# Kernel optimization log

Hardware: AMD Instinct MI355X
Metric: run time of the kernel (lower is better)

Reference implementation:

```python
import jax, jax.numpy as jnp
import numpy as np

B, L, T, D1, D2, H = 4096, 50, 100, 128, 128, 4
NUM_USERS, NUM_ITEMS = 100000, 100000
STEP = 1
NEG_INF = -9e15


def setup_inputs() -> dict:
    key = jax.random.key(0)
    ks = jax.random.split(key, 17)
    xav = lambda k, shape: jax.random.uniform(k, shape, jnp.float32,
                                              -np.sqrt(6.0 / (shape[0] + shape[1])),
                                              np.sqrt(6.0 / (shape[0] + shape[1])))
    return {
        # int inputs
        "item_seq": jax.random.randint(ks[0], (B, L), 0, NUM_ITEMS),
        "user_ids": jax.random.randint(ks[1], (B,), 0, NUM_USERS),
        "items_to_predict": jax.random.randint(ks[2], (B, T), 0, NUM_ITEMS),
        "A": jax.random.randint(ks[3], (B, L, L), 0, 2).astype(jnp.int32),
        # embedding tables (normal_(0, 1/dim) as in torch init)
        "item_emb_table": jax.random.normal(ks[4], (NUM_ITEMS, D1), jnp.float32) / D1,
        "user_emb_table": jax.random.normal(ks[5], (NUM_USERS, D2), jnp.float32) / D2,
        "W2_table": jax.random.normal(ks[6], (NUM_ITEMS, D1), jnp.float32) / D1,
        "b2_table": jnp.zeros((NUM_ITEMS, 1), jnp.float32),
        # GAT params (one head layer + output layer), xavier_uniform
        "W_att": xav(ks[7], (D1, D1)),
        "a_att": xav(ks[8], (2 * D1, 1)),
        "W_out": xav(ks[9], (D1, D1)),
        "a_out": xav(ks[10], (2 * D1, 1)),
        # item-attention MLP (torch Linear stored as [in, out] + bias)
        "att1_W": xav(ks[11], (D1, D1)),
        "att1_b": jnp.zeros((D1,), jnp.float32),
        "att2_W": xav(ks[12], (D1, H)),
        "att2_b": jnp.zeros((H,), jnp.float32),
        "user_com": xav(ks[13], (D1 + D2, D1)),
    }


def _gat_layer(x, adj, W, a, concat):
    # x: [B,L,Fin], adj: [B,L,L]
    h = jnp.einsum("blf,fg->blg", x, W)            # [B,L,F]
    F_out = W.shape[1]
    a1, a2 = a[:F_out, 0], a[F_out:, 0]
    # e[b,i,j] = tanh(h_i . a1 + h_j . a2) -- equivalent to the pairwise concat
    f1 = h @ a1                                     # [B,L]
    f2 = h @ a2                                     # [B,L]
    e = jnp.tanh(f1[:, :, None] + f2[:, None, :])   # [B,L,L]
    att = jnp.where(adj > 0, e, NEG_INF)
    att = jax.nn.softmax(att, axis=2)
    h_prime = jnp.einsum("bij,bjf->bif", att, h)
    return jax.nn.elu(h_prime) if concat else h_prime


def reference(item_seq, user_ids, items_to_predict, A,
              item_emb_table, user_emb_table, W2_table, b2_table,
              W_att, a_att, W_out, a_out,
              att1_W, att1_b, att2_W, att2_b, user_com):
    item_embs = item_emb_table[item_seq]            # [B,L,D1]
    user_emb = user_emb_table[user_ids]             # [B,D2]

    # GAT (nb_heads=1, so the head concat is identity)
    x = item_embs
    for _ in range(STEP):
        x = _gat_layer(x, A, W_att, a_att, concat=True)
        x = jax.nn.elu(_gat_layer(x, A, W_out, a_out, concat=False))
    short_embs = x                                   # [B,L,D1]

    # multi-head item attention pooling
    m1 = jnp.tanh(short_embs @ att1_W + att1_b)      # [B,L,D1]
    m2 = m1 @ att2_W + att2_b                        # [B,L,H]
    attn = jax.nn.softmax(m2, axis=2)                # softmax over heads
    matrix_z = jnp.einsum("bld,blh->bdh", short_embs, attn)  # [B,D1,H]
    attention_embs = jnp.mean(jnp.tanh(matrix_z), axis=2)     # [B,D1]

    fusion = jnp.concatenate([attention_embs, user_emb], axis=1) @ user_com  # [B,D1]

    w2 = W2_table[items_to_predict]                  # [B,T,D1]
    b2 = b2_table[items_to_predict]                  # [B,T,1]
    res = jnp.einsum("btd,bd->bt", w2, fusion) + b2[..., 0]   # baddbmm
    rel_score = jnp.einsum("bld,btd->bt", item_embs, w2)       # sum over L
    return res + rel_score
```

## Files before the change

kernel.cpp:

```cpp
#include <hip/hip_runtime.h>
#include <math.h>

#define L_  50
#define T_  100
#define NEG_INF_ -9000000000000000.0f

using bf16x8 = __attribute__((ext_vector_type(8))) short;
using f32x4 = __attribute__((ext_vector_type(4))) float;

__device__ __forceinline__ float wred_sum(float v) {
#pragma unroll
    for (int o = 32; o > 0; o >>= 1) v += __shfl_xor(v, o, 64);
    return v;
}
__device__ __forceinline__ short f2bf(float f) {
    unsigned u = __float_as_uint(f);
    return (short)((u + 0x7fffu + ((u >> 16) & 1u)) >> 16);
}
__device__ __forceinline__ unsigned short f2bfu(float f) {
    unsigned u = __float_as_uint(f);
    return (unsigned short)((u + 0x7fffu + ((u >> 16) & 1u)) >> 16);
}
__device__ __forceinline__ float bf2f(unsigned short u) {
    return __uint_as_float(((unsigned)u) << 16);
}
__device__ __forceinline__ float tanh_fast(float x) {
    const float cx = fminf(fmaxf(x, -15.f), 15.f);
    const float t = __expf(2.f * cx);
    return (t - 1.f) * __builtin_amdgcn_rcpf(t + 1.f);
}

extern "C" __global__ void __launch_bounds__(256) magnn_preswizzle(
    const float* __restrict__ W0, const float* __restrict__ W1,
    const float* __restrict__ W2, const float* __restrict__ a0,
    const float* __restrict__ a1v, unsigned short* __restrict__ out) {
    const int t = blockIdx.x * 256 + threadIdx.x;
    const int gid = t >> 6, lane = t & 63;
    if (gid >= 104) return;
    int mat, kt, nt;
    size_t base;
    if (gid < 72) {
        mat = gid / 36;
        const int rem = gid % 36;
        kt = rem / 9;
        nt = rem % 9;
        base = (size_t)mat * 18432 + (size_t)(((kt * 9 + nt) * 64 + lane) << 3);
    } else {
        mat = 2;
        const int rem = gid - 72;
        kt = rem >> 3;
        nt = rem & 7;
        base = 36864 + (size_t)(((kt * 8 + nt) * 64 + lane) << 3);
    }
    const float* Ws = (mat == 0) ? W0 : (mat == 1) ? W1 : W2;
    const int n = lane & 15;
    const int k0 = kt * 32 + (lane >> 4) * 8;
    bf16x8 v;
    if (nt < 8) {
        const int col = nt * 16 + n;
#pragma unroll
        for (int j = 0; j < 8; ++j) v[j] = f2bf(Ws[(size_t)(k0 + j) * 128 + col]);
    } else {
        if (n < 2) {
            const float* av = ((mat == 0) ? a0 : a1v) + n * 128;
#pragma unroll
            for (int j = 0; j < 8; ++j) {
                float s = 0.f;
                const float* wr = Ws + (size_t)(k0 + j) * 128;
                for (int g = 0; g < 128; ++g) s = fmaf(wr[g], av[g], s);
                v[j] = f2bf(s);
            }
        } else {
#pragma unroll
            for (int j = 0; j < 8; ++j) v[j] = 0;
        }
    }
    *(bf16x8*)(out + base) = v;
}

__device__ __forceinline__ void gemm50_gat(
    const unsigned short* __restrict__ Wb,
    const unsigned short (&xb)[50][136], unsigned short (&ht)[128][72],
    float* __restrict__ f1s, float* __restrict__ f2s, int w, int lane) {
    const int n = lane & 15, quad = lane >> 4;
    const int mrd = w * 16 + n;
    const int mr = (mrd < 50) ? mrd : 49;
    f32x4 acc[9];
#pragma unroll
    for (int nt = 0; nt < 9; ++nt) acc[nt] = (f32x4){0.f, 0.f, 0.f, 0.f};

#pragma unroll
    for (int kt = 0; kt < 4; ++kt) {
        const bf16x8 af = *(const bf16x8*)&xb[mr][kt * 32 + quad * 8];
        const unsigned short* bp = Wb + (((kt * 9) * 64 + lane) << 3);
#pragma unroll
        for (int nt = 0; nt < 9; ++nt) {
            const bf16x8 bfr = *(const bf16x8*)(bp + (nt << 9));
            acc[nt] = __builtin_amdgcn_mfma_f32_16x16x32_bf16(af, bfr, acc[nt], 0, 0, 0);
        }
    }
    const int rbase = w * 16 + quad * 4;
#pragma unroll
    for (int nt = 0; nt < 8; ++nt) {
        const int col = nt * 16 + n;
        ushort4 pk;
        pk.x = f2bfu(acc[nt][0]);
        pk.y = f2bfu(acc[nt][1]);
        pk.z = f2bfu(acc[nt][2]);
        pk.w = f2bfu(acc[nt][3]);
        *(ushort4*)&ht[col][rbase] = pk;
    }
    if (n < 2) {
        float* fs = n ? f2s : f1s;
#pragma unroll
        for (int reg = 0; reg < 4; ++reg) fs[rbase + reg] = acc[8][reg];
    }
}

__device__ __forceinline__ void gemm_m1_m2(
    const unsigned short* __restrict__ Wb, const float* __restrict__ att1_b,
    const float* __restrict__ att2_W, const float* __restrict__ att2_b,
    const unsigned short (&xb)[50][136], float* __restrict__ attn4,
    int w, int lane) {
    const int n = lane & 15, quad = lane >> 4;
    const int mrd = w * 16 + n;
    const int mr = (mrd < 50) ? mrd : 49;
    f32x4 acc[8];
#pragma unroll
    for (int nt = 0; nt < 8; ++nt) acc[nt] = (f32x4){0.f, 0.f, 0.f, 0.f};

#pragma unroll
    for (int kt = 0; kt < 4; ++kt) {
        const bf16x8 af = *(const bf16x8*)&xb[mr][kt * 32 + quad * 8];
        const unsigned short* bp = Wb + (((kt * 8) * 64 + lane) << 3);
#pragma unroll
        for (int nt = 0; nt < 8; ++nt) {
            const bf16x8 bfr = *(const bf16x8*)(bp + (nt << 9));
            acc[nt] = __builtin_amdgcn_mfma_f32_16x16x32_bf16(af, bfr, acc[nt], 0, 0, 0);
        }
    }

    float pm[4][4];
#pragma unroll
    for (int r = 0; r < 4; ++r)
#pragma unroll
        for (int h = 0; h < 4; ++h) pm[r][h] = 0.f;

#pragma unroll
    for (int nt = 0; nt < 8; ++nt) {
        const int col = nt * 16 + n;
        const float bv = att1_b[col];
        const float4 a4 = *(const float4*)&att2_W[col * 4];
#pragma unroll
        for (int r = 0; r < 4; ++r) {
            const float tv = tanh_fast(acc[nt][r] + bv);
            pm[r][0] = fmaf(tv, a4.x, pm[r][0]);
            pm[r][1] = fmaf(tv, a4.y, pm[r][1]);
            pm[r][2] = fmaf(tv, a4.z, pm[r][2]);
            pm[r][3] = fmaf(tv, a4.w, pm[r][3]);
        }
    }
#pragma unroll
    for (int r = 0; r < 4; ++r)
#pragma unroll
        for (int h = 0; h < 4; ++h) {
            float v = pm[r][h];
            v += __shfl_xor(v, 1, 64);
            v += __shfl_xor(v, 2, 64);
            v += __shfl_xor(v, 4, 64);
            v += __shfl_xor(v, 8, 64);
            pm[r][h] = v;
        }
    if (n == 0) {
        const float ab0 = att2_b[0], ab1 = att2_b[1], ab2 = att2_b[2], ab3 = att2_b[3];
        const int rbase = w * 16 + quad * 4;
#pragma unroll
        for (int r = 0; r < 4; ++r) {
            const int row = rbase + r;
            if (row < L_) {
                const float m0 = pm[r][0] + ab0, m1 = pm[r][1] + ab1;
                const float m2 = pm[r][2] + ab2, m3 = pm[r][3] + ab3;
                const float mx = fmaxf(fmaxf(m0, m1), fmaxf(m2, m3));
                const float e0 = __expf(m0 - mx), e1 = __expf(m1 - mx);
                const float e2 = __expf(m2 - mx), e3 = __expf(m3 - mx);
                const float inv = 1.f / (e0 + e1 + e2 + e3);
                *(float4*)&attn4[row * 4] =
                    make_float4(e0 * inv, e1 * inv, e2 * inv, e3 * inv);
            }
        }
    }
}

extern "C" __global__ void __launch_bounds__(256, 4) magnn_fused(
    const int* __restrict__ iseq, const int* __restrict__ uids,
    const int* __restrict__ itp, const int* __restrict__ A,
    const float* __restrict__ item_emb, const float* __restrict__ user_emb,
    const float* __restrict__ W2t, const float* __restrict__ b2t,
    const float* __restrict__ att1_b, const float* __restrict__ att2_W,
    const float* __restrict__ att2_b, const float* __restrict__ user_com,
    const unsigned short* __restrict__ Wb, float* __restrict__ out) {
    __shared__ __align__(16) unsigned short xb[50][136];
    __shared__ __align__(16) unsigned short ht[128][72];
    __shared__ __align__(16) unsigned short Pb[50][72];
    __shared__ __align__(16) float fsc[128];
    float* f1s = fsc;
    float* f2s = fsc + 64;
    float* S = (float*)&Pb[0][0];
    float* attn4 = S;
    float* cat = S + 256;
    float* fpart = S + 512;
    float* vvec = S + 640;
    float* zpart = S + 768;

    const int tid = threadIdx.x;
    const int b = blockIdx.x;
    const int w = tid >> 6, lane = tid & 63;
    const int n16 = lane & 15, quad = lane >> 4;

    const int* Ab = A + (size_t)b * (L_ * L_);
    unsigned amask = 0;
    if (lane < L_) {
#pragma unroll
        for (int k = 0; k < 13; ++k) {
            const int l = w + 4 * k;
            if (l < L_) amask |= (Ab[l * L_ + lane] > 0) ? (1u << k) : 0u;
        }
    }

    const int* isq = iseq + b * L_;
    for (int i = tid; i < L_ * 32; i += 256) {
        const int l = i >> 5, c4 = (i & 31) << 2;
        const float4 v = *(const float4*)&item_emb[(size_t)isq[l] * 128 + c4];
        ushort4 pk;
        pk.x = f2bfu(v.x); pk.y = f2bfu(v.y); pk.z = f2bfu(v.z); pk.w = f2bfu(v.w);
        *(ushort4*)&xb[l][c4] = pk;
    }
    float sval = 0.f;
    if (tid < 128) {
#pragma unroll 10
        for (int l = 0; l < L_; ++l)
            sval += item_emb[(size_t)isq[l] * 128 + tid];
    }
    __syncthreads();

#pragma unroll 1
    for (int layer = 0; layer < 2; ++layer) {
        gemm50_gat(Wb + layer * 18432, xb, ht, f1s, f2s, w, lane);
        __syncthreads();
        {
            const float f2v = (lane < L_) ? f2s[lane] : 0.f;
#pragma unroll
            for (int k = 0; k < 13; ++k) {
                const int l = w + 4 * k;
                if (l < L_) {
                    const float e = tanh_fast(f1s[l] + f2v);
                    const float p = ((amask >> k) & 1u) ? __expf(e) : 0.f;
                    Pb[l][lane] = f2bfu(p);
                }
            }
        }
        __syncthreads();
        {
            const int pm = w * 16 + n16;
            const int pmc = (pm < 50) ? pm : 49;
            const bf16x8 pa0 = *(const bf16x8*)&Pb[pmc][quad * 8];
            const bf16x8 pa1 = *(const bf16x8*)&Pb[pmc][32 + quad * 8];
            bf16x8 bones;
#pragma unroll
            for (int j = 0; j < 8; ++j)
                bones[j] = (n16 == 0) ? (short)0x3F80 : (short)0;
            f32x4 sacc = (f32x4){0.f, 0.f, 0.f, 0.f};
            sacc = __builtin_amdgcn_mfma_f32_16x16x32_bf16(pa0, bones, sacc, 0, 0, 0);
            sacc = __builtin_amdgcn_mfma_f32_16x16x32_bf16(pa1, bones, sacc, 0, 0, 0);
            f32x4 oacc[8];
#pragma unroll
            for (int nt = 0; nt < 8; ++nt) oacc[nt] = (f32x4){0.f, 0.f, 0.f, 0.f};
#pragma unroll
            for (int nt = 0; nt < 8; ++nt) {
                const bf16x8 h0 = *(const bf16x8*)&ht[nt * 16 + n16][quad * 8];
                oacc[nt] = __builtin_amdgcn_mfma_f32_16x16x32_bf16(pa0, h0, oacc[nt], 0, 0, 0);
            }
#pragma unroll
            for (int nt = 0; nt < 8; ++nt) {
                const bf16x8 h1 = *(const bf16x8*)&ht[nt * 16 + n16][32 + quad * 8];
                oacc[nt] = __builtin_amdgcn_mfma_f32_16x16x32_bf16(pa1, h1, oacc[nt], 0, 0, 0);
            }
            float rinv[4];
#pragma unroll
            for (int reg = 0; reg < 4; ++reg) {
                const float s = __shfl(sacc[reg], (lane & 48), 64);
                rinv[reg] = __builtin_amdgcn_rcpf(s);
            }
            const int rb = w * 16 + quad * 4;
#pragma unroll
            for (int nt = 0; nt < 8; ++nt) {
#pragma unroll
                for (int reg = 0; reg < 4; ++reg) {
                    const int row = rb + reg;
                    if (row < L_) {
                        float e = oacc[nt][reg] * rinv[reg];
                        e = (e > 0.f) ? e : (__expf(e) - 1.f);
                        xb[row][nt * 16 + n16] = f2bfu(e);
                    }
                }
            }
        }
        __syncthreads();
    }

    gemm_m1_m2(Wb + 36864, att1_b, att2_W, att2_b, xb, attn4, w, lane);
    __syncthreads();

    {
        const int d = tid & 127, hf2 = tid >> 7;
        float z0 = 0.f, z1 = 0.f, z2 = 0.f, z3 = 0.f;
        const int l0 = hf2 * 25;
#pragma unroll
        for (int li = 0; li < 25; ++li) {
            const int l = l0 + li;
            const float xv = bf2f(xb[l][d]);
            const float4 at = *(const float4*)&attn4[l * 4];
            z0 = fmaf(xv, at.x, z0);
            z1 = fmaf(xv, at.y, z1);
            z2 = fmaf(xv, at.z, z2);
            z3 = fmaf(xv, at.w, z3);
        }
        if (hf2) {
            zpart[0 * 128 + d] = z0;
            zpart[1 * 128 + d] = z1;
            zpart[2 * 128 + d] = z2;
            zpart[3 * 128 + d] = z3;
            cat[128 + d] = user_emb[(size_t)uids[b] * 128 + d];
        }
        __syncthreads();
        if (!hf2) {
            z0 += zpart[0 * 128 + d];
            z1 += zpart[1 * 128 + d];
            z2 += zpart[2 * 128 + d];
            z3 += zpart[3 * 128 + d];
            cat[d] = 0.25f * (tanh_fast(z0) + tanh_fast(z1) +
                              tanh_fast(z2) + tanh_fast(z3));
        }
        __syncthreads();
    }

    {
        const int g = tid & 127, hf = tid >> 7;
        const float* ucb = user_com + hf * 128 * 128 + g;
        const float* cc = cat + hf * 128;
        float acc = 0.f;
#pragma unroll 16
        for (int k = 0; k < 128; ++k) acc = fmaf(cc[k], ucb[(size_t)k * 128], acc);
        if (hf) fpart[g] = acc;
        __syncthreads();
        if (!hf) vvec[g] = acc + fpart[g] + sval;
    }
    __syncthreads();

    {
        float vv[8];
#pragma unroll
        for (int j = 0; j < 8; ++j) vv[j] = vvec[n16 * 8 + j];
        const int* itpb = itp + b * T_;
        const int tq = w * 4 + quad;
        int ti[7];
        float bv[7];
#pragma unroll
        for (int i = 0; i < 7; ++i) {
            const int t = i * 16 + tq;
            ti[i] = itpb[(t < T_) ? t : 0];
        }
#pragma unroll
        for (int i = 0; i < 7; ++i) bv[i] = b2t[ti[i]];
#pragma unroll
        for (int i = 0; i < 7; ++i) {
            const int t = i * 16 + tq;
            const float* wr = W2t + (size_t)ti[i] * 128 + n16 * 8;
            const float4 wa = *(const float4*)wr;
            const float4 wb = *(const float4*)(wr + 4);
            float r = wa.x * vv[0];
            r = fmaf(wa.y, vv[1], r);
            r = fmaf(wa.z, vv[2], r);
            r = fmaf(wa.w, vv[3], r);
            r = fmaf(wb.x, vv[4], r);
            r = fmaf(wb.y, vv[5], r);
            r = fmaf(wb.z, vv[6], r);
            r = fmaf(wb.w, vv[7], r);
            r += __shfl_xor(r, 1, 64);
            r += __shfl_xor(r, 2, 64);
            r += __shfl_xor(r, 4, 64);
            r += __shfl_xor(r, 8, 64);
            if (n16 == 0 && t < T_) out[b * T_ + t] = r + bv[i];
        }
    }
}

extern "C" void kernel_launch(void* const* d_in, const int* in_sizes, int n_in,
                              void* d_out, int out_size, void* d_ws, size_t ws_size,
                              hipStream_t stream) {
    const int* iseq = (const int*)d_in[0];
    const int* uids = (const int*)d_in[1];
    const int* itp = (const int*)d_in[2];
    const int* A = (const int*)d_in[3];
    const float* item_emb = (const float*)d_in[4];
    const float* user_emb = (const float*)d_in[5];
    const float* W2t = (const float*)d_in[6];
    const float* b2t = (const float*)d_in[7];
    const float* W_att = (const float*)d_in[8];
    const float* a_att = (const float*)d_in[9];
    const float* W_out = (const float*)d_in[10];
    const float* a_out = (const float*)d_in[11];
    const float* att1_W = (const float*)d_in[12];
    const float* att1_b = (const float*)d_in[13];
    const float* att2_W = (const float*)d_in[14];
    const float* att2_b = (const float*)d_in[15];
    const float* user_com = (const float*)d_in[16];
    float* out = (float*)d_out;
    unsigned short* Wb = (unsigned short*)d_ws;

    magnn_preswizzle<<<dim3(26), dim3(256), 0, stream>>>(W_att, W_out, att1_W,
                                                         a_att, a_out, Wb);

    const int B = in_sizes[1];
    magnn_fused<<<dim3(B), dim3(256), 0, stream>>>(
        iseq, uids, itp, A, item_emb, user_emb, W2t, b2t, att1_b, att2_W,
        att2_b, user_com, Wb, out);
}
```

Before: 359.1 us.

## Pre-transpose user_com, pack bf16 conversions, remap adjacency rows and trim syncs

The preswizzle kernel now also writes a transposed copy of user_com so the fusion matvec reads contiguous float4 rows. The a-vector projections in preswizzle are computed with a parallel shuffle reduction. In the fused kernel, bf16 conversions use the packed v_cvt_pk_bf16_f32 instruction. Each wave now owns 16 consecutive attention rows, which lets one barrier before the PV step be dropped. The z pooling and fusion stages use 128 threads without split partial sums, which removes two barriers but halves the parallelism in those stages.

Measured after the change: 460.6 us. 1.28x slower.

```diff
diff --git a/kernel.cpp b/kernel.cpp
--- a/kernel.cpp
+++ b/kernel.cpp
@@ -8,11 +8,6 @@
 using bf16x8 = __attribute__((ext_vector_type(8))) short;
 using f32x4 = __attribute__((ext_vector_type(4))) float;
 
-__device__ __forceinline__ float wred_sum(float v) {
-#pragma unroll
-    for (int o = 32; o > 0; o >>= 1) v += __shfl_xor(v, o, 64);
-    return v;
-}
 __device__ __forceinline__ short f2bf(float f) {
     unsigned u = __float_as_uint(f);
     return (short)((u + 0x7fffu + ((u >> 16) & 1u)) >> 16);
@@ -23,6 +18,11 @@
 }
 __device__ __forceinline__ float bf2f(unsigned short u) {
     return __uint_as_float(((unsigned)u) << 16);
+}
+__device__ __forceinline__ unsigned cvt_pk_bf16(float lo, float hi) {
+    unsigned r;
+    asm("v_cvt_pk_bf16_f32 %0, %1, %2" : "=v"(r) : "v"(lo), "v"(hi));
+    return r;
 }
 __device__ __forceinline__ float tanh_fast(float x) {
     const float cx = fminf(fmaxf(x, -15.f), 15.f);
@@ -33,10 +33,26 @@
 extern "C" __global__ void __launch_bounds__(256) magnn_preswizzle(
     const float* __restrict__ W0, const float* __restrict__ W1,
     const float* __restrict__ W2, const float* __restrict__ a0,
-    const float* __restrict__ a1v, unsigned short* __restrict__ out) {
+    const float* __restrict__ a1v, const float* __restrict__ user_com,
+    unsigned short* __restrict__ out, float* __restrict__ ucT) {
     const int t = blockIdx.x * 256 + threadIdx.x;
     const int gid = t >> 6, lane = t & 63;
-    if (gid >= 104) return;
+    if (gid >= 136) return;
+    if (gid >= 104) {
+        const int r = gid - 104;
+#pragma unroll
+        for (int rep = 0; rep < 4; ++rep) {
+            const int c = r * 64 + lane + rep * 2048;
+            const int g = c >> 6, k4 = (c & 63) << 2;
+            float4 v;
+            v.x = user_com[(size_t)(k4 + 0) * 128 + g];
+            v.y = user_com[(size_t)(k4 + 1) * 128 + g];
+            v.z = user_com[(size_t)(k4 + 2) * 128 + g];
+            v.w = user_com[(size_t)(k4 + 3) * 128 + g];
+            *(float4*)&ucT[(size_t)g * 256 + k4] = v;
+        }
+        return;
+    }
     int mat, kt, nt;
     size_t base;
     if (gid < 72) {
@@ -61,18 +77,22 @@
 #pragma unroll
         for (int j = 0; j < 8; ++j) v[j] = f2bf(Ws[(size_t)(k0 + j) * 128 + col]);
     } else {
-        if (n < 2) {
-            const float* av = ((mat == 0) ? a0 : a1v) + n * 128;
-#pragma unroll
-            for (int j = 0; j < 8; ++j) {
-                float s = 0.f;
-                const float* wr = Ws + (size_t)(k0 + j) * 128;
-                for (int g = 0; g < 128; ++g) s = fmaf(wr[g], av[g], s);
-                v[j] = f2bf(s);
-            }
-        } else {
-#pragma unroll
-            for (int j = 0; j < 8; ++j) v[j] = 0;
+        const float* avb = (mat == 0) ? a0 : a1v;
+#pragma unroll
+        for (int j = 0; j < 8; ++j) v[j] = 0;
+#pragma unroll
+        for (int pv = 0; pv < 16; ++pv) {
+            const int j = pv & 7, vec = pv >> 3;
+            const float* wr = Ws + (size_t)(k0 + j) * 128 + n * 8;
+            const float* av = avb + vec * 128 + n * 8;
+            float s = 0.f;
+#pragma unroll
+            for (int g = 0; g < 8; ++g) s = fmaf(wr[g], av[g], s);
+            s += __shfl_xor(s, 1, 16);
+            s += __shfl_xor(s, 2, 16);
+            s += __shfl_xor(s, 4, 16);
+            s += __shfl_xor(s, 8, 16);
+            if (n == vec) v[j] = f2bf(s);
         }
     }
     *(bf16x8*)(out + base) = v;
@@ -103,12 +123,10 @@
 #pragma unroll
     for (int nt = 0; nt < 8; ++nt) {
         const int col = nt * 16 + n;
-        ushort4 pk;
-        pk.x = f2bfu(acc[nt][0]);
-        pk.y = f2bfu(acc[nt][1]);
-        pk.z = f2bfu(acc[nt][2]);
-        pk.w = f2bfu(acc[nt][3]);
-        *(ushort4*)&ht[col][rbase] = pk;
+        uint2 pk;
+        pk.x = cvt_pk_bf16(acc[nt][0], acc[nt][1]);
+        pk.y = cvt_pk_bf16(acc[nt][2], acc[nt][3]);
+        *(uint2*)&ht[col][rbase] = pk;
     }
     if (n < 2) {
         float* fs = n ? f2s : f1s;
@@ -197,8 +215,8 @@
     const float* __restrict__ item_emb, const float* __restrict__ user_emb,
     const float* __restrict__ W2t, const float* __restrict__ b2t,
     const float* __restrict__ att1_b, const float* __restrict__ att2_W,
-    const float* __restrict__ att2_b, const float* __restrict__ user_com,
-    const unsigned short* __restrict__ Wb, float* __restrict__ out) {
+    const float* __restrict__ att2_b, const unsigned short* __restrict__ Wb,
+    const float* __restrict__ ucT, float* __restrict__ out) {
     __shared__ __align__(16) unsigned short xb[50][136];
     __shared__ __align__(16) unsigned short ht[128][72];
     __shared__ __align__(16) unsigned short Pb[50][72];
@@ -208,9 +226,7 @@
     float* S = (float*)&Pb[0][0];
     float* attn4 = S;
     float* cat = S + 256;
-    float* fpart = S + 512;
-    float* vvec = S + 640;
-    float* zpart = S + 768;
+    float* vvec = S + 512;
 
     const int tid = threadIdx.x;
     const int b = blockIdx.x;
@@ -221,8 +237,8 @@
     unsigned amask = 0;
     if (lane < L_) {
 #pragma unroll
-        for (int k = 0; k < 13; ++k) {
-            const int l = w + 4 * k;
+        for (int k = 0; k < 16; ++k) {
+            const int l = w * 16 + k;
             if (l < L_) amask |= (Ab[l * L_ + lane] > 0) ? (1u << k) : 0u;
         }
     }
@@ -231,9 +247,10 @@
     for (int i = tid; i < L_ * 32; i += 256) {
         const int l = i >> 5, c4 = (i & 31) << 2;
         const float4 v = *(const float4*)&item_emb[(size_t)isq[l] * 128 + c4];
-        ushort4 pk;
-        pk.x = f2bfu(v.x); pk.y = f2bfu(v.y); pk.z = f2bfu(v.z); pk.w = f2bfu(v.w);
-        *(ushort4*)&xb[l][c4] = pk;
+        uint2 pk;
+        pk.x = cvt_pk_bf16(v.x, v.y);
+        pk.y = cvt_pk_bf16(v.z, v.w);
+        *(uint2*)&xb[l][c4] = pk;
     }
     float sval = 0.f;
     if (tid < 128) {
@@ -250,8 +267,8 @@
         {
             const float f2v = (lane < L_) ? f2s[lane] : 0.f;
 #pragma unroll
-            for (int k = 0; k < 13; ++k) {
-                const int l = w + 4 * k;
+            for (int k = 0; k < 16; ++k) {
+                const int l = w * 16 + k;
                 if (l < L_) {
                     const float e = tanh_fast(f1s[l] + f2v);
                     const float p = ((amask >> k) & 1u) ? __expf(e) : 0.f;
@@ -259,7 +276,6 @@
                 }
             }
         }
-        __syncthreads();
         {
             const int pm = w * 16 + n16;
             const int pmc = (pm < 50) ? pm : 49;
@@ -294,15 +310,19 @@
             const int rb = w * 16 + quad * 4;
 #pragma unroll
             for (int nt = 0; nt < 8; ++nt) {
+                float ev[4];
 #pragma unroll
                 for (int reg = 0; reg < 4; ++reg) {
-                    const int row = rb + reg;
-                    if (row < L_) {
-                        float e = oacc[nt][reg] * rinv[reg];
-                        e = (e > 0.f) ? e : (__expf(e) - 1.f);
-                        xb[row][nt * 16 + n16] = f2bfu(e);
-                    }
+                    const float e = oacc[nt][reg] * rinv[reg];
+                    ev[reg] = (e > 0.f) ? e : (__expf(e) - 1.f);
                 }
+                const unsigned q0 = cvt_pk_bf16(ev[0], ev[1]);
+                const unsigned q1 = cvt_pk_bf16(ev[2], ev[3]);
+                const int c = nt * 16 + n16;
+                if (rb + 0 < L_) xb[rb + 0][c] = (unsigned short)(q0 & 0xffffu);
+                if (rb + 1 < L_) xb[rb + 1][c] = (unsigned short)(q0 >> 16);
+                if (rb + 2 < L_) xb[rb + 2][c] = (unsigned short)(q1 & 0xffffu);
+                if (rb + 3 < L_) xb[rb + 3][c] = (unsigned short)(q1 >> 16);
             }
         }
         __syncthreads();
@@ -311,13 +331,11 @@
     gemm_m1_m2(Wb + 36864, att1_b, att2_W, att2_b, xb, attn4, w, lane);
     __syncthreads();
 
-    {
-        const int d = tid & 127, hf2 = tid >> 7;
+    if (tid < 128) {
+        const int d = tid;
         float z0 = 0.f, z1 = 0.f, z2 = 0.f, z3 = 0.f;
-        const int l0 = hf2 * 25;
-#pragma unroll
-        for (int li = 0; li < 25; ++li) {
-            const int l = l0 + li;
+#pragma unroll 5
+        for (int l = 0; l < L_; ++l) {
             const float xv = bf2f(xb[l][d]);
             const float4 at = *(const float4*)&attn4[l * 4];
             z0 = fmaf(xv, at.x, z0);
@@ -325,42 +343,32 @@
             z2 = fmaf(xv, at.z, z2);
             z3 = fmaf(xv, at.w, z3);
         }
-        if (hf2) {
-            zpart[0 * 128 + d] = z0;
-            zpart[1 * 128 + d] = z1;
-            zpart[2 * 128 + d] = z2;
-            zpart[3 * 128 + d] = z3;
-            cat[128 + d] = user_emb[(size_t)uids[b] * 128 + d];
-        }
-        __syncthreads();
-        if (!hf2) {
-            z0 += zpart[0 * 128 + d];
-            z1 += zpart[1 * 128 + d];
-            z2 += zpart[2 * 128 + d];
-            z3 += zpart[3 * 128 + d];
-            cat[d] = 0.25f * (tanh_fast(z0) + tanh_fast(z1) +
-                              tanh_fast(z2) + tanh_fast(z3));
-        }
-        __syncthreads();
-    }
+        cat[d] = 0.25f * (tanh_fast(z0) + tanh_fast(z1) +
+                          tanh_fast(z2) + tanh_fast(z3));
+    } else {
+        cat[tid] = user_emb[(size_t)uids[b] * 128 + (tid - 128)];
+    }
+    __syncthreads();
+
+    if (tid < 128) {
+        const float* ur = ucT + (size_t)tid * 256;
+        float acc = 0.f;
+#pragma unroll
+        for (int k4 = 0; k4 < 64; ++k4) {
+            const float4 cv = *(const float4*)&cat[k4 * 4];
+            const float4 uv = *(const float4*)&ur[k4 * 4];
+            acc = fmaf(cv.x, uv.x, acc);
+            acc = fmaf(cv.y, uv.y, acc);
+            acc = fmaf(cv.z, uv.z, acc);
+            acc = fmaf(cv.w, uv.w, acc);
+        }
+        vvec[tid] = acc + sval;
+    }
+    __syncthreads();
 
     {
-        const int g = tid & 127, hf = tid >> 7;
-        const float* ucb = user_com + hf * 128 * 128 + g;
-        const float* cc = cat + hf * 128;
-        float acc = 0.f;
-#pragma unroll 16
-        for (int k = 0; k < 128; ++k) acc = fmaf(cc[k], ucb[(size_t)k * 128], acc);
-        if (hf) fpart[g] = acc;
-        __syncthreads();
-        if (!hf) vvec[g] = acc + fpart[g] + sval;
-    }
-    __syncthreads();
-
-    {
-        float vv[8];
-#pragma unroll
-        for (int j = 0; j < 8; ++j) vv[j] = vvec[n16 * 8 + j];
+        const float4 vva = *(const float4*)&vvec[n16 * 8];
+        const float4 vvb = *(const float4*)&vvec[n16 * 8 + 4];
         const int* itpb = itp + b * T_;
         const int tq = w * 4 + quad;
         int ti[7];
@@ -378,14 +386,14 @@
             const float* wr = W2t + (size_t)ti[i] * 128 + n16 * 8;
             const float4 wa = *(const float4*)wr;
             const float4 wb = *(const float4*)(wr + 4);
-            float r = wa.x * vv[0];
-            r = fmaf(wa.y, vv[1], r);
-            r = fmaf(wa.z, vv[2], r);
-            r = fmaf(wa.w, vv[3], r);
-            r = fmaf(wb.x, vv[4], r);
-            r = fmaf(wb.y, vv[5], r);
-            r = fmaf(wb.z, vv[6], r);
-            r = fmaf(wb.w, vv[7], r);
+            float r = wa.x * vva.x;
+            r = fmaf(wa.y, vva.y, r);
+            r = fmaf(wa.z, vva.z, r);
+            r = fmaf(wa.w, vva.w, r);
+            r = fmaf(wb.x, vvb.x, r);
+            r = fmaf(wb.y, vvb.y, r);
+            r = fmaf(wb.z, vvb.z, r);
+            r = fmaf(wb.w, vvb.w, r);
             r += __shfl_xor(r, 1, 64);
             r += __shfl_xor(r, 2, 64);
             r += __shfl_xor(r, 4, 64);
@@ -417,12 +425,13 @@
     const float* user_com = (const float*)d_in[16];
     float* out = (float*)d_out;
     unsigned short* Wb = (unsigned short*)d_ws;
-
-    magnn_preswizzle<<<dim3(26), dim3(256), 0, stream>>>(W_att, W_out, att1_W,
-                                                         a_att, a_out, Wb);
+    float* ucT = (float*)((char*)d_ws + 106496);
+
+    magnn_preswizzle<<<dim3(34), dim3(256), 0, stream>>>(
+        W_att, W_out, att1_W, a_att, a_out, user_com, Wb, ucT);
 
     const int B = in_sizes[1];
     magnn_fused<<<dim3(B), dim3(256), 0, stream>>>(
         iseq, uids, itp, A, item_emb, user_emb, W2t, b2t, att1_b, att2_W,
-        att2_b, user_com, Wb, out);
-}
+        att2_b, Wb, ucT, out);
+}
```

## Remap attention rows to own-warp tiles, drop barrier, split gathers and preswizzle dots

Applied to the files above, without the earlier changes.

Each warp now computes the masked exp scores for the same 16 rows it later consumes as an MFMA A-tile. That lets the barrier between writing Pb and reading it be removed. The sum of item embeddings over L is split across all 256 threads with a shared partial buffer, and the preswizzle a-vector dot products are spread across 16 lanes with shuffles instead of one lane doing 128-long loops. The final vvec read uses float4 loads. Relying on intra-warp ordering for Pb without a barrier risks a race on LDS visibility, and warp 3 handles only 2 valid rows, so the work is imbalanced.

Measured after the change: 409.1 us. +13.9%, slower.

```diff
diff --git a/kernel.cpp b/kernel.cpp
--- a/kernel.cpp
+++ b/kernel.cpp
@@ -8,11 +8,6 @@
 using bf16x8 = __attribute__((ext_vector_type(8))) short;
 using f32x4 = __attribute__((ext_vector_type(4))) float;
 
-__device__ __forceinline__ float wred_sum(float v) {
-#pragma unroll
-    for (int o = 32; o > 0; o >>= 1) v += __shfl_xor(v, o, 64);
-    return v;
-}
 __device__ __forceinline__ short f2bf(float f) {
     unsigned u = __float_as_uint(f);
     return (short)((u + 0x7fffu + ((u >> 16) & 1u)) >> 16);
@@ -61,18 +56,22 @@
 #pragma unroll
         for (int j = 0; j < 8; ++j) v[j] = f2bf(Ws[(size_t)(k0 + j) * 128 + col]);
     } else {
-        if (n < 2) {
-            const float* av = ((mat == 0) ? a0 : a1v) + n * 128;
-#pragma unroll
-            for (int j = 0; j < 8; ++j) {
-                float s = 0.f;
-                const float* wr = Ws + (size_t)(k0 + j) * 128;
-                for (int g = 0; g < 128; ++g) s = fmaf(wr[g], av[g], s);
-                v[j] = f2bf(s);
-            }
-        } else {
-#pragma unroll
-            for (int j = 0; j < 8; ++j) v[j] = 0;
+        const float* avb = (mat == 0) ? a0 : a1v;
+#pragma unroll
+        for (int j = 0; j < 8; ++j) v[j] = 0;
+#pragma unroll
+        for (int pv = 0; pv < 16; ++pv) {
+            const int j = pv & 7, vec = pv >> 3;
+            const float* wr = Ws + (size_t)(k0 + j) * 128 + n * 8;
+            const float* av = avb + vec * 128 + n * 8;
+            float s = 0.f;
+#pragma unroll
+            for (int g = 0; g < 8; ++g) s = fmaf(wr[g], av[g], s);
+            s += __shfl_xor(s, 1, 16);
+            s += __shfl_xor(s, 2, 16);
+            s += __shfl_xor(s, 4, 16);
+            s += __shfl_xor(s, 8, 16);
+            if (n == vec) v[j] = f2bf(s);
         }
     }
     *(bf16x8*)(out + base) = v;
@@ -203,6 +202,7 @@
     __shared__ __align__(16) unsigned short ht[128][72];
     __shared__ __align__(16) unsigned short Pb[50][72];
     __shared__ __align__(16) float fsc[128];
+    __shared__ __align__(16) float spart[128];
     float* f1s = fsc;
     float* f2s = fsc + 64;
     float* S = (float*)&Pb[0][0];
@@ -221,8 +221,8 @@
     unsigned amask = 0;
     if (lane < L_) {
 #pragma unroll
-        for (int k = 0; k < 13; ++k) {
-            const int l = w + 4 * k;
+        for (int k = 0; k < 16; ++k) {
+            const int l = w * 16 + k;
             if (l < L_) amask |= (Ab[l * L_ + lane] > 0) ? (1u << k) : 0u;
         }
     }
@@ -236,10 +236,15 @@
         *(ushort4*)&xb[l][c4] = pk;
     }
     float sval = 0.f;
-    if (tid < 128) {
-#pragma unroll 10
-        for (int l = 0; l < L_; ++l)
-            sval += item_emb[(size_t)isq[l] * 128 + tid];
+    {
+        const int d = tid & 127, hf2 = tid >> 7;
+        const int l0 = hf2 * 25;
+        float s = 0.f;
+#pragma unroll 5
+        for (int l = l0; l < l0 + 25; ++l)
+            s += item_emb[(size_t)isq[l] * 128 + d];
+        if (hf2) spart[d] = s;
+        else sval = s;
     }
     __syncthreads();
 
@@ -250,8 +255,8 @@
         {
             const float f2v = (lane < L_) ? f2s[lane] : 0.f;
 #pragma unroll
-            for (int k = 0; k < 13; ++k) {
-                const int l = w + 4 * k;
+            for (int k = 0; k < 16; ++k) {
+                const int l = w * 16 + k;
                 if (l < L_) {
                     const float e = tanh_fast(f1s[l] + f2v);
                     const float p = ((amask >> k) & 1u) ? __expf(e) : 0.f;
@@ -259,7 +264,6 @@
                 }
             }
         }
-        __syncthreads();
         {
             const int pm = w * 16 + n16;
             const int pmc = (pm < 50) ? pm : 49;
@@ -353,14 +357,13 @@
         for (int k = 0; k < 128; ++k) acc = fmaf(cc[k], ucb[(size_t)k * 128], acc);
         if (hf) fpart[g] = acc;
         __syncthreads();
-        if (!hf) vvec[g] = acc + fpart[g] + sval;
+        if (!hf) vvec[g] = acc + fpart[g] + sval + spart[g];
     }
     __syncthreads();
 
     {
-        float vv[8];
-#pragma unroll
-        for (int j = 0; j < 8; ++j) vv[j] = vvec[n16 * 8 + j];
+        const float4 vva = *(const float4*)&vvec[n16 * 8];
+        const float4 vvb = *(const float4*)&vvec[n16 * 8 + 4];
         const int* itpb = itp + b * T_;
         const int tq = w * 4 + quad;
         int ti[7];
@@ -378,14 +381,14 @@
             const float* wr = W2t + (size_t)ti[i] * 128 + n16 * 8;
             const float4 wa = *(const float4*)wr;
             const float4 wb = *(const float4*)(wr + 4);
-            float r = wa.x * vv[0];
-            r = fmaf(wa.y, vv[1], r);
-            r = fmaf(wa.z, vv[2], r);
-            r = fmaf(wa.w, vv[3], r);
-            r = fmaf(wb.x, vv[4], r);
-            r = fmaf(wb.y, vv[5], r);
-            r = fmaf(wb.z, vv[6], r);
-            r = fmaf(wb.w, vv[7], r);
+            float r = wa.x * vva.x;
+            r = fmaf(wa.y, vva.y, r);
+            r = fmaf(wa.z, vva.z, r);
+            r = fmaf(wa.w, vva.w, r);
+            r = fmaf(wb.x, vvb.x, r);
+            r = fmaf(wb.y, vvb.y, r);
+            r = fmaf(wb.z, vvb.z, r);
+            r = fmaf(wb.w, vvb.w, r);
             r += __shfl_xor(r, 1, 64);
             r += __shfl_xor(r, 2, 64);
             r += __shfl_xor(r, 4, 64);
```
